# Kernel tuning notes

Hardware: AMD Instinct MI355X
Metric: run time of the kernel (lower is better)

The kernel has to match this reference:

```python
import jax, jax.numpy as jnp
import numpy as np

N_NODES = 50000
N_EDGES = 600000
DIN, DH, DOUT = 128, 256, 128
BN_EPS = 1e-5
LRELU_SLOPE = 0.01


def setup_inputs() -> dict:
    key = jax.random.key(0)
    ks = jax.random.split(key, 16)
    rn = lambda k, s, sc=0.05: jax.random.normal(k, s, dtype=jnp.float32) * sc
    return {
        'nodes': jax.random.normal(ks[0], (N_NODES, DIN), dtype=jnp.float32),
        'src': jax.random.randint(ks[1], (N_EDGES,), 0, N_NODES, dtype=jnp.int32),
        'dst': jax.random.randint(ks[2], (N_EDGES,), 0, N_NODES, dtype=jnp.int32),
        # FeedForward params
        'Wf1': rn(ks[3], (DIN, DH)), 'bf1': jnp.zeros((DH,), jnp.float32),
        'gf1': jnp.ones((DH,), jnp.float32), 'bef1': jnp.zeros((DH,), jnp.float32),
        'Wf2': rn(ks[4], (DH, DIN)), 'bf2': jnp.zeros((DIN,), jnp.float32),
        'gf2': jnp.ones((DIN,), jnp.float32), 'bef2': jnp.zeros((DIN,), jnp.float32),
        # SAGEConv 1 (in->hidden)
        'Ws1': rn(ks[5], (DIN, DH)), 'Wn1': rn(ks[6], (DIN, DH)), 'b1': jnp.zeros((DH,), jnp.float32),
        'gs1': jnp.ones((DH,), jnp.float32), 'bs1': jnp.zeros((DH,), jnp.float32),
        # SAGEConv 2 (hidden->out)
        'Ws2': rn(ks[7], (DH, DOUT)), 'Wn2': rn(ks[8], (DH, DOUT)), 'b2': jnp.zeros((DOUT,), jnp.float32),
        'gs2': jnp.ones((DOUT,), jnp.float32), 'bs2': jnp.zeros((DOUT,), jnp.float32),
    }


def _bn(x, gamma, beta):
    # BatchNorm1d, training mode: batch stats over node dim, biased variance
    mu = jnp.mean(x, axis=0)
    var = jnp.mean(jnp.square(x - mu), axis=0)
    return (x - mu) * jax.lax.rsqrt(var + BN_EPS) * gamma + beta


def _sage_mean(x, src, dst, Wself, Wneigh, bias):
    # DGL SAGEConv('mean'): out = x@Wself + mean_{src->dst}(x[src])@Wneigh + bias
    n = x.shape[0]
    deg = jax.ops.segment_sum(jnp.ones_like(src, dtype=x.dtype), dst, num_segments=n)
    agg = jax.ops.segment_sum(x[src], dst, num_segments=n)  # [N, d] irregular scatter-add
    h_neigh = agg / jnp.maximum(deg, 1.0)[:, None]
    return x @ Wself + h_neigh @ Wneigh + bias


def reference(nodes, src, dst, Wf1, bf1, gf1, bef1, Wf2, bf2, gf2, bef2,
              Ws1, Wn1, b1, gs1, bs1, Ws2, Wn2, b2, gs2, bs2):
    # FeedForward (dropout=0 -> identity)
    h = jax.nn.relu(_bn(nodes @ Wf1 + bf1, gf1, bef1))
    h = jax.nn.relu(_bn(h @ Wf2 + bf2, gf2, bef2))
    # SAGE layer 1
    h1 = _sage_mean(h, src, dst, Ws1, Wn1, b1)
    h1 = jax.nn.leaky_relu(_bn(h1, gs1, bs1), LRELU_SLOPE)
    # SAGE layer 2
    h2 = _sage_mean(h1, src, dst, Ws2, Wn2, b2)
    return jax.nn.leaky_relu(_bn(h2, gs2, bs2), LRELU_SLOPE)
```

## Files before the change

### kernel.cpp

```cpp
#include <hip/hip_runtime.h>

#define DIN 128
#define BN_EPS 1e-5f

typedef __attribute__((ext_vector_type(8))) short bf16x8;
typedef __attribute__((ext_vector_type(8))) unsigned short us8;
typedef __attribute__((ext_vector_type(4))) float f32x4;

__device__ __forceinline__ ushort f2bf(float f) {
    unsigned u = __float_as_uint(f);
    u += 0x7fffu + ((u >> 16) & 1u);
    return (ushort)(u >> 16);
}
__device__ __forceinline__ float bf2f(ushort h) {
    return __uint_as_float(((unsigned)h) << 16);
}
__device__ __forceinline__ f32x4 asf4(us8 v) {
    union { us8 u; f32x4 f; } x; x.u = v; return x.f;
}

template<int KC, int NT, int LOGNG, int STATS, int BNIN>
__global__ __launch_bounds__(256) void gemm_lds(
    const ushort* __restrict__ A, const ushort* __restrict__ BT,
    ushort* __restrict__ C, int mStrips, int N,
    float* __restrict__ gsums, float* __restrict__ gsqs,
    const float* __restrict__ isums, const float* __restrict__ isqs,
    const float* __restrict__ igam, const float* __restrict__ ibet,
    float invM, float negSlope,
    const ushort* __restrict__ A2)
{
    constexpr int K = KC * 32;
    constexpr int CPR = KC * 4;
    constexpr int LOGCPR = (KC == 4) ? 4 : 5;
    constexpr int LPL = KC / 4;
    constexpr int LPL2 = (BNIN == 3) ? 2 * LPL : LPL;
    __shared__ ushort abuf[2][16 * K];

    int tid = threadIdx.x;
    int lane = tid & 63;
    int w = tid >> 6;
    int cl = lane & 15, q = lane >> 4;
    int grp = blockIdx.x & ((1 << LOGNG) - 1);
    int s0 = blockIdx.x >> LOGNG;
    int TT = gridDim.x >> LOGNG;
    int colBase = grp * (4 * 16 * NT) + w * (16 * NT);
    int chBase = w * (16 * KC);

    bf16x8 bf[NT][KC];
    #pragma unroll
    for (int nt = 0; nt < NT; nt++) {
        const ushort* bp = BT + (long)(colBase + nt * 16 + cl) * K + q * 8;
        #pragma unroll
        for (int kc = 0; kc < KC; kc++)
            bf[nt][kc] = *(const bf16x8*)(bp + kc * 32);
    }

    float sc8[8], sh8[8];
    const ushort* dsrc = A;
    int dcol = 0;
    if (BNIN == 1) {
        int cb = ((chBase + lane) & (CPR - 1)) * 8;
        #pragma unroll
        for (int e = 0; e < 8; e++) {
            float mean = isums[cb + e] * invM;
            float var = isqs[cb + e] * invM - mean * mean;
            float s = igam[cb + e] * rsqrtf(var + BN_EPS);
            sc8[e] = s;
            sh8[e] = ibet[cb + e] - mean * s;
        }
    } else if (BNIN == 2) {
        int c = (chBase + lane) & (CPR - 1);
        dsrc = (c < 16) ? A : A2;
        dcol = (c & 15) * 8;
        if (c < 16) {
            int cb = c * 8;
            #pragma unroll
            for (int e = 0; e < 8; e++) {
                float mean = isums[cb + e] * invM;
                float var = isqs[cb + e] * invM - mean * mean;
                float s = igam[cb + e] * rsqrtf(var + BN_EPS);
                sc8[e] = s;
                sh8[e] = ibet[cb + e] - mean * s;
            }
        } else {
            #pragma unroll
            for (int e = 0; e < 8; e++) { sc8[e] = 1.0f; sh8[e] = 0.0f; }
        }
    }

    float ssum[NT], ssq[NT];
    #pragma unroll
    for (int nt = 0; nt < NT; nt++) { ssum[nt] = 0.f; ssq[nt] = 0.f; }

    auto stage_load = [&](us8 (&stg)[LPL2], int strip) {
        if (BNIN == 3) {
            const float* Af = (const float*)A;
            #pragma unroll
            for (int u = 0; u < LPL; u++) {
                int ch = chBase + u * 64 + lane;
                int r = ch >> LOGCPR;
                int c = ch & (CPR - 1);
                const float* p = Af + (long)(strip * 16 + r) * K + c * 8;
                stg[2 * u]     = *(const us8*)p;
                stg[2 * u + 1] = *(const us8*)(p + 4);
            }
        } else if (BNIN == 2) {
            #pragma unroll
            for (int u = 0; u < LPL; u++) {
                int r = (chBase + u * 64 + lane) >> LOGCPR;
                stg[u] = *(const us8*)(dsrc + ((long)(strip * 16 + r)) * 128 + dcol);
            }
        } else {
            const ushort* As = A + (long)strip * 16 * K;
            #pragma unroll
            for (int u = 0; u < LPL; u++)
                stg[u] = *(const us8*)(As + (chBase + u * 64 + lane) * 8);
        }
    };
    auto stage_write = [&](int buf, us8 (&stg)[LPL2]) {
        #pragma unroll
        for (int u = 0; u < LPL; u++) {
            int ch = chBase + u * 64 + lane;
            int r = ch >> LOGCPR;
            int c = ch & (CPR - 1);
            us8 v;
            if (BNIN == 3) {
                f32x4 lo = asf4(stg[2 * u]);
                f32x4 hi = asf4(stg[2 * u + 1]);
                us8 o;
                o[0] = f2bf(lo[0]); o[1] = f2bf(lo[1]); o[2] = f2bf(lo[2]); o[3] = f2bf(lo[3]);
                o[4] = f2bf(hi[0]); o[5] = f2bf(hi[1]); o[6] = f2bf(hi[2]); o[7] = f2bf(hi[3]);
                v = o;
            } else {
                v = stg[u];
                if (BNIN == 1 || BNIN == 2) {
                    us8 o;
                    #pragma unroll
                    for (int e = 0; e < 8; e++) {
                        float f = bf2f(v[e]) * sc8[e] + sh8[e];
                        f = (f > 0.f) ? f : f * negSlope;
                        o[e] = f2bf(f);
                    }
                    v = o;
                }
            }
            *(us8*)(abuf[buf] + (((r << LOGCPR) + (c ^ (r & 7))) * 8)) = v;
        }
    };

    us8 stgA[LPL2], stgB[LPL2];
    int s = s0;
    stage_load(stgA, s);
    if (s + TT < mStrips) stage_load(stgB, s + TT);
    stage_write(0, stgA);
    if (s + 2 * TT < mStrips) stage_load(stgA, s + 2 * TT);
    __syncthreads();
    int cur = 0;

#define GEMM_STEP(STG)                                                                  \
    {                                                                                   \
        bf16x8 af[KC];                                                                  \
        _Pragma("unroll")                                                               \
        for (int kc = 0; kc < KC; kc++)                                                 \
            af[kc] = *(const bf16x8*)(abuf[cur] +                                       \
                     (((cl << LOGCPR) + ((kc * 4 + q) ^ (cl & 7))) * 8));               \
        if (s + TT < mStrips) stage_write(cur ^ 1, STG);                                \
        if (s + 3 * TT < mStrips) stage_load(STG, s + 3 * TT);                          \
        f32x4 acc[NT] = {};                                                             \
        _Pragma("unroll")                                                               \
        for (int kc = 0; kc < KC; kc++)                                                 \
            _Pragma("unroll")                                                           \
            for (int nt = 0; nt < NT; nt++)                                             \
                acc[nt] = __builtin_amdgcn_mfma_f32_16x16x32_bf16(af[kc], bf[nt][kc],   \
                                                                  acc[nt], 0, 0, 0);    \
        int rowBase = s * 16;                                                           \
        _Pragma("unroll")                                                               \
        for (int nt = 0; nt < NT; nt++) {                                               \
            _Pragma("unroll")                                                           \
            for (int r = 0; r < 4; r++) {                                               \
                float v = acc[nt][r];                                                   \
                long row = rowBase + q * 4 + r;                                         \
                C[row * N + colBase + nt * 16 + cl] = f2bf(v);                          \
                if (STATS) { ssum[nt] += v; ssq[nt] += v * v; }                         \
            }                                                                           \
        }                                                                               \
        __syncthreads();                                                                \
        s += TT; cur ^= 1;                                                              \
    }

    while (true) {
        GEMM_STEP(stgB);
        if (s >= mStrips) break;
        GEMM_STEP(stgA);
        if (s >= mStrips) break;
    }
#undef GEMM_STEP

    if (STATS) {
        #pragma unroll
        for (int nt = 0; nt < NT; nt++) {
            ssum[nt] += __shfl_xor(ssum[nt], 16, 64);
            ssum[nt] += __shfl_xor(ssum[nt], 32, 64);
            ssq[nt]  += __shfl_xor(ssq[nt], 16, 64);
            ssq[nt]  += __shfl_xor(ssq[nt], 32, 64);
        }
        if (q == 0) {
            #pragma unroll
            for (int nt = 0; nt < NT; nt++) {
                atomicAdd(&gsums[colBase + nt * 16 + cl], ssum[nt]);
                atomicAdd(&gsqs[colBase + nt * 16 + cl], ssq[nt]);
            }
        }
    }
}

__global__ __launch_bounds__(256) void setup_all(
    const float* __restrict__ W0, const float* __restrict__ W1,
    const float* __restrict__ W2, const float* __restrict__ W3,
    const float* __restrict__ W4, const float* __restrict__ W5,
    ushort* __restrict__ WT,
    int* __restrict__ zeroInts, int nZero4, int nbZero,
    float* __restrict__ stats)
{
    int b = blockIdx.x;
    int tid = threadIdx.x;
    if (b < 768) {
        int seg = b >> 7;
        const float* W; int logK, dstBase, stride, kOff;
        switch (seg) {
            case 0: W = W0; logK = 7; dstBase = 0;      stride = 128; kOff = 0;   break;
            case 1: W = W1; logK = 8; dstBase = 32768;  stride = 256; kOff = 0;   break;
            case 2: W = W2; logK = 7; dstBase = 65536;  stride = 256; kOff = 0;   break;
            case 3: W = W3; logK = 7; dstBase = 65536;  stride = 256; kOff = 128; break;
            case 4: W = W4; logK = 8; dstBase = 131072; stride = 256; kOff = 0;   break;
            default:W = W5; logK = 8; dstBase = 163840; stride = 256; kOff = 0;   break;
        }
        int t = (b & 127) * 256 + tid;
        int N = 32768 >> logK;
        int k = t & ((1 << logK) - 1);
        int n = t >> logK;
        WT[(long)dstBase + (long)n * stride + kOff + k] = f2bf(W[(long)k * N + n]);
        return;
    }
    b -= 768;
    if (b < nbZero) {
        int t = b * 256 + tid;
        if (t < nZero4) *(int4*)&zeroInts[(long)t * 4] = make_int4(0, 0, 0, 0);
        return;
    }
    b -= nbZero;
    int t = b * 256 + tid;
    if (t < 512) *(float4*)&stats[(long)t * 4] = make_float4(0, 0, 0, 0);
}

__global__ __launch_bounds__(256) void bnact_f32(
    float* __restrict__ X,
    const float* __restrict__ sums, const float* __restrict__ sqs,
    const float* __restrict__ gamma, const float* __restrict__ beta, float invM,
    int nRows, float negSlope)
{
    __shared__ float ssc[128], ssh[128];
    int tid = threadIdx.x;
    if (tid < 128) {
        float mean = sums[tid] * invM;
        float var = sqs[tid] * invM - mean * mean;
        float sc = gamma[tid] * rsqrtf(var + BN_EPS);
        ssc[tid] = sc;
        ssh[tid] = beta[tid] - mean * sc;
    }
    __syncthreads();
    int cb = (tid * 4) & 127;
    float4 sc = *(const float4*)&ssc[cb];
    float4 sh = *(const float4*)&ssh[cb];
    int r0 = blockIdx.x * 8 + ((tid * 4) >> 7);
    int rstride = gridDim.x * 8;
    for (int row = r0; row < nRows; row += rstride) {
        float4 v = *(const float4*)&X[(long)row * 128 + cb];
        float a = v.x * sc.x + sh.x; a = (a > 0.f) ? a : a * negSlope;
        float b = v.y * sc.y + sh.y; b = (b > 0.f) ? b : b * negSlope;
        float d = v.z * sc.z + sh.z; d = (d > 0.f) ? d : d * negSlope;
        float e = v.w * sc.w + sh.w; e = (e > 0.f) ? e : e * negSlope;
        *(float4*)&X[(long)row * 128 + cb] = make_float4(a, b, d, e);
    }
}

__global__ __launch_bounds__(256) void colstats128(
    const float* __restrict__ X, float* __restrict__ sums, float* __restrict__ sqs, int M)
{
    __shared__ float ss[128], sq[128];
    int tid = threadIdx.x;
    if (tid < 128) { ss[tid] = 0.f; sq[tid] = 0.f; }
    __syncthreads();
    int cg = tid & 31;
    int worker = (blockIdx.x << 3) | (tid >> 5);
    int totalW = gridDim.x << 3;
    float4 s4 = make_float4(0, 0, 0, 0), q4 = make_float4(0, 0, 0, 0);
    for (int r = worker; r < M; r += totalW) {
        float4 v = *(const float4*)&X[(long)r * 128 + cg * 4];
        s4.x += v.x; s4.y += v.y; s4.z += v.z; s4.w += v.w;
        q4.x += v.x * v.x; q4.y += v.y * v.y; q4.z += v.z * v.z; q4.w += v.w * v.w;
    }
    atomicAdd(&ss[cg * 4 + 0], s4.x); atomicAdd(&sq[cg * 4 + 0], q4.x);
    atomicAdd(&ss[cg * 4 + 1], s4.y); atomicAdd(&sq[cg * 4 + 1], q4.y);
    atomicAdd(&ss[cg * 4 + 2], s4.z); atomicAdd(&sq[cg * 4 + 2], q4.z);
    atomicAdd(&ss[cg * 4 + 3], s4.w); atomicAdd(&sq[cg * 4 + 3], q4.w);
    __syncthreads();
    if (tid < 128) { atomicAdd(&sums[tid], ss[tid]); atomicAdd(&sqs[tid], sq[tid]); }
}

__global__ void degcount_kernel(const int* __restrict__ dst, int* __restrict__ degi, int E)
{
    int i = blockIdx.x * blockDim.x + threadIdx.x;
    if (i < E) atomicAdd(&degi[dst[i]], 1);
}

__global__ __launch_bounds__(256) void scan_block_sums(const int* __restrict__ degi,
                                                       int* __restrict__ partial, int n)
{
    __shared__ int s[256];
    int i = blockIdx.x * 256 + threadIdx.x;
    s[threadIdx.x] = (i < n) ? degi[i] : 0;
    __syncthreads();
    for (int off = 128; off > 0; off >>= 1) {
        if (threadIdx.x < off) s[threadIdx.x] += s[threadIdx.x + off];
        __syncthreads();
    }
    if (threadIdx.x == 0) partial[blockIdx.x] = s[0];
}

__global__ __launch_bounds__(256) void scan_final(const int* __restrict__ degi,
                                                  const int* __restrict__ partial,
                                                  int* __restrict__ rowstart, int n, int nb)
{
    __shared__ int s[256];
    __shared__ int ps[256];
    int tid = threadIdx.x;
    ps[tid] = (tid < nb && tid < (int)blockIdx.x) ? partial[tid] : 0;
    __syncthreads();
    for (int off = 128; off > 0; off >>= 1) {
        if (tid < off) ps[tid] += ps[tid + off];
        __syncthreads();
    }
    int offset = ps[0];
    int i = blockIdx.x * 256 + tid;
    int v = (i < n) ? degi[i] : 0;
    s[tid] = v;
    __syncthreads();
    for (int off = 1; off < 256; off <<= 1) {
        int t = (tid >= off) ? s[tid - off] : 0;
        __syncthreads();
        s[tid] += t;
        __syncthreads();
    }
    if (i < n) rowstart[i] = offset + s[tid] - v;
}

__global__ void fillcsr_kernel(const int* __restrict__ src, const int* __restrict__ dst,
                               const int* __restrict__ rowstart, int* __restrict__ cursor,
                               int* __restrict__ csr, int E)
{
    int i = blockIdx.x * blockDim.x + threadIdx.x;
    if (i < E) {
        int d = dst[i];
        int p = atomicAdd(&cursor[d], 1);
        csr[rowstart[d] + p] = src[i];
    }
}

__global__ __launch_bounds__(256) void gather16_bn(
    const ushort* __restrict__ X, const int* __restrict__ rowstart,
    const int* __restrict__ degi, const int* __restrict__ csr,
    ushort* __restrict__ AGG, int nN,
    const float* __restrict__ isums, const float* __restrict__ isqs,
    const float* __restrict__ igam, const float* __restrict__ ibet, float invM)
{
    int wv = (blockIdx.x * blockDim.x + threadIdx.x) >> 6;
    int lane = threadIdx.x & 63;
    if (wv >= nN) return;
    int g = lane >> 4;
    int sc = lane & 15;
    float sc8[8], sh8[8];
    {
        int cb = sc * 8;
        #pragma unroll
        for (int e = 0; e < 8; e++) {
            float mean = isums[cb + e] * invM;
            float var = isqs[cb + e] * invM - mean * mean;
            float s = igam[cb + e] * rsqrtf(var + BN_EPS);
            sc8[e] = s;
            sh8[e] = ibet[cb + e] - mean * s;
        }
    }
    int start = rowstart[wv], d = degi[wv];
    const ushort* Xc = X + sc * 8;
    float acc[8] = {};
    auto accbn8 = [&](us8 v) {
        #pragma unroll
        for (int e = 0; e < 8; e++)
            acc[e] += fmaxf(bf2f(v[e]) * sc8[e] + sh8[e], 0.f);
    };
    if (d > 0) {
        int dm = (d < 64) ? d : 64;
        int idx_l = csr[start + ((lane < dm) ? lane : (dm - 1))];
        int j = 0;
        for (; j + 8 <= dm; j += 8) {
            int i0 = __shfl(idx_l, j + g, 64);
            int i1 = __shfl(idx_l, j + 4 + g, 64);
            us8 v0 = *(const us8*)(Xc + (long)i0 * 128);
            us8 v1 = *(const us8*)(Xc + (long)i1 * 128);
            accbn8(v0);
            accbn8(v1);
        }
        if (j + 4 <= dm) {
            int i0 = __shfl(idx_l, j + g, 64);
            us8 v0 = *(const us8*)(Xc + (long)i0 * 128);
            accbn8(v0);
            j += 4;
        }
        int rem = dm - j;
        if (rem > 0) {
            int sl = j + ((g < rem) ? g : (rem - 1));
            int i0 = __shfl(idx_l, sl, 64);
            if (g < rem) {
                us8 v0 = *(const us8*)(Xc + (long)i0 * 128);
                accbn8(v0);
            }
        }
        for (int jj = 64; jj < d; jj += 4) {
            if (jj + g < d) {
                int i0 = csr[start + jj + g];
                us8 v0 = *(const us8*)(Xc + (long)i0 * 128);
                accbn8(v0);
            }
        }
    }
    #pragma unroll
    for (int e = 0; e < 8; e++) {
        acc[e] += __shfl_xor(acc[e], 16, 64);
        acc[e] += __shfl_xor(acc[e], 32, 64);
    }
    if (g == 0) {
        float inv = 1.f / fmaxf((float)d, 1.f);
        us8 o;
        #pragma unroll
        for (int e = 0; e < 8; e++) o[e] = f2bf(acc[e] * inv);
        *(us8*)(AGG + (long)wv * 128 + sc * 8) = o;
    }
}

__device__ __forceinline__ void acc8(float acc[8], us8 v) {
    #pragma unroll
    for (int e = 0; e < 8; e++) acc[e] += bf2f(v[e]);
}

__global__ __launch_bounds__(256) void gather16_fuse(
    const ushort* __restrict__ Z, const int* __restrict__ rowstart,
    const int* __restrict__ degi, const int* __restrict__ csr,
    float* __restrict__ O, int nN)
{
    int wv = (blockIdx.x * blockDim.x + threadIdx.x) >> 6;
    int lane = threadIdx.x & 63;
    if (wv >= nN) return;
    int g = lane >> 4;
    int sc = lane & 15;
    int start = rowstart[wv], d = degi[wv];
    const ushort* Zc = Z + sc * 8;
    us8 selfv = *(const us8*)(Zc + (long)wv * 256 + 128);
    float acc[8] = {};
    if (d > 0) {
        int dm = (d < 64) ? d : 64;
        int idx_l = csr[start + ((lane < dm) ? lane : (dm - 1))];
        int j = 0;
        for (; j + 8 <= dm; j += 8) {
            int i0 = __shfl(idx_l, j + g, 64);
            int i1 = __shfl(idx_l, j + 4 + g, 64);
            us8 v0 = *(const us8*)(Zc + (long)i0 * 256);
            us8 v1 = *(const us8*)(Zc + (long)i1 * 256);
            acc8(acc, v0);
            acc8(acc, v1);
        }
        if (j + 4 <= dm) {
            int i0 = __shfl(idx_l, j + g, 64);
            us8 v0 = *(const us8*)(Zc + (long)i0 * 256);
            acc8(acc, v0);
            j += 4;
        }
        int rem = dm - j;
        if (rem > 0) {
            int sl = j + ((g < rem) ? g : (rem - 1));
            int i0 = __shfl(idx_l, sl, 64);
            if (g < rem) {
                us8 v0 = *(const us8*)(Zc + (long)i0 * 256);
                acc8(acc, v0);
            }
        }
        for (int jj = 64; jj < d; jj += 4) {
            if (jj + g < d) {
                int i0 = csr[start + jj + g];
                us8 v0 = *(const us8*)(Zc + (long)i0 * 256);
                acc8(acc, v0);
            }
        }
    }
    #pragma unroll
    for (int e = 0; e < 8; e++) {
        acc[e] += __shfl_xor(acc[e], 16, 64);
        acc[e] += __shfl_xor(acc[e], 32, 64);
    }
    if (g == 0) {
        float inv = 1.f / fmaxf((float)d, 1.f);
        float r[8];
        #pragma unroll
        for (int e = 0; e < 8; e++) r[e] = acc[e] * inv + bf2f(selfv[e]);
        float* op = O + (long)wv * 128 + sc * 8;
        *(float4*)op = make_float4(r[0], r[1], r[2], r[3]);
        *(float4*)(op + 4) = make_float4(r[4], r[5], r[6], r[7]);
    }
}

extern "C" void kernel_launch(void* const* d_in, const int* in_sizes, int n_in,
                              void* d_out, int out_size, void* d_ws, size_t ws_size,
                              hipStream_t stream)
{
    const float* nodes = (const float*)d_in[0];
    const int*   src   = (const int*)d_in[1];
    const int*   dst   = (const int*)d_in[2];
    const float* Wf1   = (const float*)d_in[3];
    const float* gf1   = (const float*)d_in[5];
    const float* bef1  = (const float*)d_in[6];
    const float* Wf2   = (const float*)d_in[7];
    const float* gf2   = (const float*)d_in[9];
    const float* bef2  = (const float*)d_in[10];
    const float* Ws1   = (const float*)d_in[11];
    const float* Wn1   = (const float*)d_in[12];
    const float* gs1   = (const float*)d_in[14];
    const float* bs1   = (const float*)d_in[15];
    const float* Ws2   = (const float*)d_in[16];
    const float* Wn2   = (const float*)d_in[17];
    const float* gs2   = (const float*)d_in[19];
    const float* bs2   = (const float*)d_in[20];

    int nN = in_sizes[0] / DIN;
    int nE = in_sizes[1];
    float* out = (float*)d_out;
    int mStrips = nN / 16;
    float invM = 1.0f / nN;

    ushort* PRE = (ushort*)d_ws;
    ushort* BF1 = PRE + (size_t)nN * 256;
    ushort* BF2 = BF1 + (size_t)nN * 256;
    float* stats = (float*)(BF2 + (size_t)nN * 256);
    float* scale = stats + 2048;
    float* shift = scale + 256;
    ushort* WT   = (ushort*)(shift + 256);
    int* degi     = (int*)(WT + 196608);
    int* cursor   = degi + nN;
    int* rowstart = cursor + nN;
    int* partial  = rowstart + nN;
    int* csr      = partial + 256;

    ushort* Wf1T = WT;
    ushort* Wf2T = WT + 32768;
    ushort* Wc1T = WT + 65536;
    ushort* Wc2T = WT + 131072;
    ushort* AGG  = BF2;

    dim3 blk(256);
    auto cdiv = [](int a, int b) { return (a + b - 1) / b; };
    int nScanBlocks = cdiv(nN, 256);

    int nZero4 = (2 * nN) / 4;
    int nbZero = cdiv(nZero4, 256);
    setup_all<<<dim3(768 + nbZero + 2), blk, 0, stream>>>(
        Wf1, Wf2, Ws1, Wn1, Wn2, Ws2, WT,
        degi, nZero4, nbZero, stats);

    degcount_kernel<<<dim3(cdiv(nE, 256)), blk, 0, stream>>>(dst, degi, nE);
    scan_block_sums<<<dim3(nScanBlocks), blk, 0, stream>>>(degi, partial, nN);
    scan_final<<<dim3(nScanBlocks), blk, 0, stream>>>(degi, partial, rowstart, nN, nScanBlocks);
    fillcsr_kernel<<<dim3(cdiv(nE, 256)), blk, 0, stream>>>(src, dst, rowstart, cursor, csr, nE);

    gemm_lds<4, 4, 0, 1, 3><<<dim3(512), blk, 0, stream>>>(
        (const ushort*)nodes, Wf1T, PRE, mStrips, 256, stats, stats + 256,
        nullptr, nullptr, nullptr, nullptr, 0.f, 0.f, nullptr);

    gemm_lds<8, 2, 0, 1, 1><<<dim3(512), blk, 0, stream>>>(
        PRE, Wf2T, BF1, mStrips, 128, stats + 512, stats + 768,
        stats, stats + 256, gf1, bef1, invM, 0.0f, nullptr);

    gather16_bn<<<dim3(cdiv(nN * 64, 256)), blk, 0, stream>>>(
        BF1, rowstart, degi, csr, AGG, nN,
        stats + 512, stats + 768, gf2, bef2, invM);

    gemm_lds<8, 4, 0, 1, 2><<<dim3(512), blk, 0, stream>>>(
        BF1, Wc1T, PRE, mStrips, 256, stats + 1024, stats + 1280,
        stats + 512, stats + 768, gf2, bef2, invM, 0.0f, AGG);

    gemm_lds<8, 4, 0, 0, 1><<<dim3(512), blk, 0, stream>>>(
        PRE, Wc2T, BF2, mStrips, 256, nullptr, nullptr,
        stats + 1024, stats + 1280, gs1, bs1, invM, 0.01f, nullptr);

    gather16_fuse<<<dim3(cdiv(nN * 64, 256)), blk, 0, stream>>>(BF2, rowstart, degi, csr, out, nN);

    colstats128<<<dim3(240), blk, 0, stream>>>(out, stats + 1536, stats + 1792, nN);
    bnact_f32<<<dim3(2048), blk, 0, stream>>>(out, stats + 1536, stats + 1792, gs2, bs2, invM,
                                              nN, 0.01f);
}
```

Before: 343.1 us.

## Fold degree count and CSR scans into setup and FF GEMM launches

The degree-count atomics move into the setup_all launch as extra blocks. The two scan phases, block sums and the final prefix, ride as extra blocks appended to the two feed-forward GEMM launches, and the int zeroing is replaced by hipMemsetAsync. This removes three separate kernel launches and lets the small scan work overlap with the GEMM blocks. In exchange the GEMM kernels carry an extra branch and extra shared memory, and the order in which scan and GEMM blocks run within each launch is left to the scheduler.

```diff
diff --git a/kernel.cpp b/kernel.cpp
--- a/kernel.cpp
+++ b/kernel.cpp
@@ -19,16 +19,56 @@
     union { us8 u; f32x4 f; } x; x.u = v; return x.f;
 }
 
-template<int KC, int NT, int LOGNG, int STATS, int BNIN>
+template<int KC, int NT, int LOGNG, int STATS, int BNIN, int EXTRA>
 __global__ __launch_bounds__(256) void gemm_lds(
     const ushort* __restrict__ A, const ushort* __restrict__ BT,
-    ushort* __restrict__ C, int mStrips, int N,
+    ushort* __restrict__ C, int mStrips, int N, int gemmBlocks,
     float* __restrict__ gsums, float* __restrict__ gsqs,
     const float* __restrict__ isums, const float* __restrict__ isqs,
     const float* __restrict__ igam, const float* __restrict__ ibet,
     float invM, float negSlope,
-    const ushort* __restrict__ A2)
-{
+    const ushort* __restrict__ A2,
+    const int* __restrict__ sc_degi, int* __restrict__ sc_partial,
+    int* __restrict__ sc_rowstart, int sc_n, int sc_nb)
+{
+    int tid = threadIdx.x;
+
+    if (EXTRA != 0 && (int)blockIdx.x >= gemmBlocks) {
+        __shared__ int xs[256];
+        __shared__ int xps[256];
+        int b = blockIdx.x - gemmBlocks;
+        if (EXTRA == 1) {
+            int i = b * 256 + tid;
+            xs[tid] = (i < sc_n) ? sc_degi[i] : 0;
+            __syncthreads();
+            for (int off = 128; off > 0; off >>= 1) {
+                if (tid < off) xs[tid] += xs[tid + off];
+                __syncthreads();
+            }
+            if (tid == 0) sc_partial[b] = xs[0];
+        } else {
+            xps[tid] = (tid < sc_nb && tid < b) ? sc_partial[tid] : 0;
+            __syncthreads();
+            for (int off = 128; off > 0; off >>= 1) {
+                if (tid < off) xps[tid] += xps[tid + off];
+                __syncthreads();
+            }
+            int offset = xps[0];
+            int i = b * 256 + tid;
+            int v = (i < sc_n) ? sc_degi[i] : 0;
+            xs[tid] = v;
+            __syncthreads();
+            for (int off = 1; off < 256; off <<= 1) {
+                int t = (tid >= off) ? xs[tid - off] : 0;
+                __syncthreads();
+                xs[tid] += t;
+                __syncthreads();
+            }
+            if (i < sc_n) sc_rowstart[i] = offset + xs[tid] - v;
+        }
+        return;
+    }
+
     constexpr int K = KC * 32;
     constexpr int CPR = KC * 4;
     constexpr int LOGCPR = (KC == 4) ? 4 : 5;
@@ -36,13 +76,12 @@
     constexpr int LPL2 = (BNIN == 3) ? 2 * LPL : LPL;
     __shared__ ushort abuf[2][16 * K];
 
-    int tid = threadIdx.x;
     int lane = tid & 63;
     int w = tid >> 6;
     int cl = lane & 15, q = lane >> 4;
     int grp = blockIdx.x & ((1 << LOGNG) - 1);
     int s0 = blockIdx.x >> LOGNG;
-    int TT = gridDim.x >> LOGNG;
+    int TT = gemmBlocks >> LOGNG;
     int colBase = grp * (4 * 16 * NT) + w * (16 * NT);
     int chBase = w * (16 * KC);
 
@@ -219,8 +258,8 @@
     const float* __restrict__ W2, const float* __restrict__ W3,
     const float* __restrict__ W4, const float* __restrict__ W5,
     ushort* __restrict__ WT,
-    int* __restrict__ zeroInts, int nZero4, int nbZero,
-    float* __restrict__ stats)
+    float* __restrict__ stats,
+    const int* __restrict__ dst, int* __restrict__ degi, int E)
 {
     int b = blockIdx.x;
     int tid = threadIdx.x;
@@ -243,14 +282,14 @@
         return;
     }
     b -= 768;
-    if (b < nbZero) {
+    if (b < 2) {
         int t = b * 256 + tid;
-        if (t < nZero4) *(int4*)&zeroInts[(long)t * 4] = make_int4(0, 0, 0, 0);
+        if (t < 512) *(float4*)&stats[(long)t * 4] = make_float4(0, 0, 0, 0);
         return;
     }
-    b -= nbZero;
-    int t = b * 256 + tid;
-    if (t < 512) *(float4*)&stats[(long)t * 4] = make_float4(0, 0, 0, 0);
+    b -= 2;
+    int i = b * 256 + tid;
+    if (i < E) atomicAdd(&degi[dst[i]], 1);
 }
 
 __global__ __launch_bounds__(256) void bnact_f32(
@@ -306,53 +345,6 @@
     atomicAdd(&ss[cg * 4 + 3], s4.w); atomicAdd(&sq[cg * 4 + 3], q4.w);
     __syncthreads();
     if (tid < 128) { atomicAdd(&sums[tid], ss[tid]); atomicAdd(&sqs[tid], sq[tid]); }
-}
-
-__global__ void degcount_kernel(const int* __restrict__ dst, int* __restrict__ degi, int E)
-{
-    int i = blockIdx.x * blockDim.x + threadIdx.x;
-    if (i < E) atomicAdd(&degi[dst[i]], 1);
-}
-
-__global__ __launch_bounds__(256) void scan_block_sums(const int* __restrict__ degi,
-                                                       int* __restrict__ partial, int n)
-{
-    __shared__ int s[256];
-    int i = blockIdx.x * 256 + threadIdx.x;
-    s[threadIdx.x] = (i < n) ? degi[i] : 0;
-    __syncthreads();
-    for (int off = 128; off > 0; off >>= 1) {
-        if (threadIdx.x < off) s[threadIdx.x] += s[threadIdx.x + off];
-        __syncthreads();
-    }
-    if (threadIdx.x == 0) partial[blockIdx.x] = s[0];
-}
-
-__global__ __launch_bounds__(256) void scan_final(const int* __restrict__ degi,
-                                                  const int* __restrict__ partial,
-                                                  int* __restrict__ rowstart, int n, int nb)
-{
-    __shared__ int s[256];
-    __shared__ int ps[256];
-    int tid = threadIdx.x;
-    ps[tid] = (tid < nb && tid < (int)blockIdx.x) ? partial[tid] : 0;
-    __syncthreads();
-    for (int off = 128; off > 0; off >>= 1) {
-        if (tid < off) ps[tid] += ps[tid + off];
-        __syncthreads();
-    }
-    int offset = ps[0];
-    int i = blockIdx.x * 256 + tid;
-    int v = (i < n) ? degi[i] : 0;
-    s[tid] = v;
-    __syncthreads();
-    for (int off = 1; off < 256; off <<= 1) {
-        int t = (tid >= off) ? s[tid - off] : 0;
-        __syncthreads();
-        s[tid] += t;
-        __syncthreads();
-    }
-    if (i < n) rowstart[i] = offset + s[tid] - v;
 }
 
 __global__ void fillcsr_kernel(const int* __restrict__ src, const int* __restrict__ dst,
@@ -568,37 +560,38 @@
     dim3 blk(256);
     auto cdiv = [](int a, int b) { return (a + b - 1) / b; };
     int nScanBlocks = cdiv(nN, 256);
-
-    int nZero4 = (2 * nN) / 4;
-    int nbZero = cdiv(nZero4, 256);
-    setup_all<<<dim3(768 + nbZero + 2), blk, 0, stream>>>(
-        Wf1, Wf2, Ws1, Wn1, Wn2, Ws2, WT,
-        degi, nZero4, nbZero, stats);
-
-    degcount_kernel<<<dim3(cdiv(nE, 256)), blk, 0, stream>>>(dst, degi, nE);
-    scan_block_sums<<<dim3(nScanBlocks), blk, 0, stream>>>(degi, partial, nN);
-    scan_final<<<dim3(nScanBlocks), blk, 0, stream>>>(degi, partial, rowstart, nN, nScanBlocks);
-    fillcsr_kernel<<<dim3(cdiv(nE, 256)), blk, 0, stream>>>(src, dst, rowstart, cursor, csr, nE);
-
-    gemm_lds<4, 4, 0, 1, 3><<<dim3(512), blk, 0, stream>>>(
-        (const ushort*)nodes, Wf1T, PRE, mStrips, 256, stats, stats + 256,
-        nullptr, nullptr, nullptr, nullptr, 0.f, 0.f, nullptr);
-
-    gemm_lds<8, 2, 0, 1, 1><<<dim3(512), blk, 0, stream>>>(
-        PRE, Wf2T, BF1, mStrips, 128, stats + 512, stats + 768,
-        stats, stats + 256, gf1, bef1, invM, 0.0f, nullptr);
+    int nbE = cdiv(nE, 256);
+
+    hipMemsetAsync(degi, 0, 2 * (size_t)nN * sizeof(int), stream);
+
+    setup_all<<<dim3(768 + 2 + nbE), blk, 0, stream>>>(
+        Wf1, Wf2, Ws1, Wn1, Wn2, Ws2, WT, stats, dst, degi, nE);
+
+    gemm_lds<4, 4, 0, 1, 3, 1><<<dim3(512 + nScanBlocks), blk, 0, stream>>>(
+        (const ushort*)nodes, Wf1T, PRE, mStrips, 256, 512, stats, stats + 256,
+        nullptr, nullptr, nullptr, nullptr, 0.f, 0.f, nullptr,
+        degi, partial, nullptr, nN, 0);
+
+    gemm_lds<8, 2, 0, 1, 1, 2><<<dim3(512 + nScanBlocks), blk, 0, stream>>>(
+        PRE, Wf2T, BF1, mStrips, 128, 512, stats + 512, stats + 768,
+        stats, stats + 256, gf1, bef1, invM, 0.0f, nullptr,
+        degi, partial, rowstart, nN, nScanBlocks);
+
+    fillcsr_kernel<<<dim3(nbE), blk, 0, stream>>>(src, dst, rowstart, cursor, csr, nE);
 
     gather16_bn<<<dim3(cdiv(nN * 64, 256)), blk, 0, stream>>>(
         BF1, rowstart, degi, csr, AGG, nN,
         stats + 512, stats + 768, gf2, bef2, invM);
 
-    gemm_lds<8, 4, 0, 1, 2><<<dim3(512), blk, 0, stream>>>(
-        BF1, Wc1T, PRE, mStrips, 256, stats + 1024, stats + 1280,
-        stats + 512, stats + 768, gf2, bef2, invM, 0.0f, AGG);
-
-    gemm_lds<8, 4, 0, 0, 1><<<dim3(512), blk, 0, stream>>>(
-        PRE, Wc2T, BF2, mStrips, 256, nullptr, nullptr,
-        stats + 1024, stats + 1280, gs1, bs1, invM, 0.01f, nullptr);
+    gemm_lds<8, 4, 0, 1, 2, 0><<<dim3(512), blk, 0, stream>>>(
+        BF1, Wc1T, PRE, mStrips, 256, 512, stats + 1024, stats + 1280,
+        stats + 512, stats + 768, gf2, bef2, invM, 0.0f, AGG,
+        nullptr, nullptr, nullptr, 0, 0);
+
+    gemm_lds<8, 4, 0, 0, 1, 0><<<dim3(512), blk, 0, stream>>>(
+        PRE, Wc2T, BF2, mStrips, 256, 512, nullptr, nullptr,
+        stats + 1024, stats + 1280, gs1, bs1, invM, 0.01f, nullptr,
+        nullptr, nullptr, nullptr, 0, 0);
 
     gather16_fuse<<<dim3(cdiv(nN * 64, 256)), blk, 0, stream>>>(BF2, rowstart, degi, csr, out, nN);
 
```

New measurement: 339.8 us. Within noise of the previous version (-1.0%).
